# Kernel optimization log

Hardware: AMD Instinct MI355X
Metric: run time of the kernel (lower is better)

Reference implementation:

```python
import jax, jax.numpy as jnp
import numpy as np

# SCC (sliding/overlapping channel convolution) config, matching init_kwargs
C_IN = 64
C_OUT = 64
GRP_N = 8
OVERLAP = 4
G = C_IN // GRP_N          # input_grp_unit_dim = channels per sliding window = 8
STEP = G - OVERLAP         # channel stride between consecutive output channels = 4
B, H, W = 32, 128, 128


def setup_inputs() -> dict:
    key = jax.random.key(0)
    k1, k2 = jax.random.split(key)
    x = jax.random.normal(k1, (B, C_IN, H, W), dtype=jnp.float32)
    stdv = 1.0 / np.sqrt(G)  # reset_parameters: uniform(-stdv, stdv)
    weights = jax.random.uniform(k2, (C_OUT, G), dtype=jnp.float32,
                                 minval=-stdv, maxval=stdv)
    return {"x": x, "weights": weights}


def _expand_weights(weights):
    # Scatter the (C_OUT, G) sliding-window weights into a dense (C_OUT, C_IN)
    # channel-mixing matrix. Output channel o reads input channels
    # (o*STEP + j) % C_IN for j in [0, G). This keeps the irregular channel
    # access as a tiny scatter instead of materializing a (B,O,G,H,W) gather.
    o = jnp.arange(C_OUT)[:, None]            # (C_OUT, 1)
    j = jnp.arange(G)[None, :]                # (1, G)
    idx = (o * STEP + j) % C_IN               # (C_OUT, G) wrap-around window
    w_full = jnp.zeros((C_OUT, C_IN), dtype=weights.dtype)
    w_full = w_full.at[jnp.broadcast_to(o, idx.shape), idx].add(weights)
    return w_full


def reference(x, weights):
    w_full = _expand_weights(weights)                 # (C_OUT, C_IN)
    # 1x1 spatial conv == per-pixel channel contraction
    return jnp.einsum('oc,bchw->bohw', w_full, x)     # (B, C_OUT, H, W)
```

## Files before the change

kernel.cpp:

```cpp
#include <hip/hip_runtime.h>
#include <hip/hip_bf16.h>


#define CIN   64
#define COUT  64
#define GW    8
#define STEP  4
#define HW4   4096

__global__ __launch_bounds__(256) void scc_kernel(
    const float4* __restrict__ x,
    const float*  __restrict__ w,
    float4* __restrict__ out)
{
    __shared__ float4 wsv[COUT * 2];
    {
        float* ws = (float*)wsv;
        for (int i = threadIdx.x; i < COUT * GW; i += blockDim.x)
            ws[i] = w[i];
    }
    __syncthreads();

    int t   = blockIdx.x * blockDim.x + threadIdx.x;
    int b   = t >> 12;
    int hw4 = t & (HW4 - 1);

    const float4* xp = x   + ((long)b * CIN) * HW4 + hw4;
    float4*       op = out + ((long)b * COUT) * HW4 + hw4;

    float4 win[8];
#pragma unroll
    for (int k = 0; k < 8; ++k)
        win[k] = xp[(long)k * HW4];

#pragma unroll
    for (int wi = 0; wi < 16; ++wi) {
        float4 nxt[4];
        if (wi < 15) {
#pragma unroll
            for (int k = 0; k < 4; ++k) {
                int c = (4 * wi + 8 + k) & (CIN - 1);
                nxt[k] = xp[(long)c * HW4];
            }
        }

#pragma unroll
        for (int q = 0; q < 4; ++q) {
            int o = wi + 16 * q;
            float4 w0 = wsv[o * 2 + 0];
            float4 w1 = wsv[o * 2 + 1];
            float4 a;
            a.x = 0.f; a.y = 0.f; a.z = 0.f; a.w = 0.f;
#pragma unroll
            for (int j = 0; j < 8; ++j) {
                float wt = (j < 4) ? ((const float*)&w0)[j]
                                   : ((const float*)&w1)[j - 4];
                float4 xv = win[(4 * wi + j) & 7];
                a.x = fmaf(wt, xv.x, a.x);
                a.y = fmaf(wt, xv.y, a.y);
                a.z = fmaf(wt, xv.z, a.z);
                a.w = fmaf(wt, xv.w, a.w);
            }
            op[(long)o * HW4] = a;
        }

        if (wi < 15) {
#pragma unroll
            for (int k = 0; k < 4; ++k)
                win[(4 * wi + 8 + k) & 7] = nxt[k];
        }
    }
}

extern "C" void kernel_launch(void* const* d_in, const int* in_sizes, int n_in,
                              void* d_out, int out_size, void* d_ws, size_t ws_size,
                              hipStream_t stream) {
    const float4* x = (const float4*)d_in[0];
    const float*  w = (const float*)d_in[1];
    float4* out     = (float4*)d_out;

    const int total_vec = 32 * HW4;
    const int block = 256;
    const int grid  = total_vec / block;

    scc_kernel<<<grid, block, 0, stream>>>(x, w, out);
}
```

Before: 48.71 us.

## Split each pixel's output channels across four threads to raise parallelism

```diff
diff --git a/kernel.cpp b/kernel.cpp
--- a/kernel.cpp
+++ b/kernel.cpp
@@ -5,7 +5,6 @@
 #define CIN   64
 #define COUT  64
 #define GW    8
-#define STEP  4
 #define HW4   4096
 
 __global__ __launch_bounds__(256) void scc_kernel(
@@ -13,48 +12,44 @@
     const float*  __restrict__ w,
     float4* __restrict__ out)
 {
-    __shared__ float4 wsv[COUT * 2];
-    {
-        float* ws = (float*)wsv;
-        for (int i = threadIdx.x; i < COUT * GW; i += blockDim.x)
-            ws[i] = w[i];
-    }
+    __shared__ float ws[COUT * GW];
+    for (int i = threadIdx.x; i < COUT * GW; i += blockDim.x)
+        ws[i] = w[i];
     __syncthreads();
 
-    int t   = blockIdx.x * blockDim.x + threadIdx.x;
-    int b   = t >> 12;
-    int hw4 = t & (HW4 - 1);
+    const int tid = threadIdx.x;
+    const int q0  = tid >> 6;
+    const int pi  = blockIdx.x * 64 + (tid & 63);
+    const int b   = pi >> 12;
+    const int hw4 = pi & (HW4 - 1);
 
     const float4* xp = x   + ((long)b * CIN) * HW4 + hw4;
     float4*       op = out + ((long)b * COUT) * HW4 + hw4;
 
+    const int cbase = 16 * q0;
+
     float4 win[8];
 #pragma unroll
     for (int k = 0; k < 8; ++k)
-        win[k] = xp[(long)k * HW4];
+        win[k] = xp[(long)((cbase + k) & (CIN - 1)) * HW4];
 
 #pragma unroll
-    for (int wi = 0; wi < 16; ++wi) {
+    for (int wi = 0; wi < 4; ++wi) {
         float4 nxt[4];
-        if (wi < 15) {
+        if (wi < 3) {
 #pragma unroll
-            for (int k = 0; k < 4; ++k) {
-                int c = (4 * wi + 8 + k) & (CIN - 1);
-                nxt[k] = xp[(long)c * HW4];
-            }
+            for (int k = 0; k < 4; ++k)
+                nxt[k] = xp[(long)((cbase + 4 * wi + 8 + k) & (CIN - 1)) * HW4];
         }
 
 #pragma unroll
         for (int q = 0; q < 4; ++q) {
-            int o = wi + 16 * q;
-            float4 w0 = wsv[o * 2 + 0];
-            float4 w1 = wsv[o * 2 + 1];
+            int o = 4 * q0 + wi + 16 * q;
             float4 a;
             a.x = 0.f; a.y = 0.f; a.z = 0.f; a.w = 0.f;
 #pragma unroll
             for (int j = 0; j < 8; ++j) {
-                float wt = (j < 4) ? ((const float*)&w0)[j]
-                                   : ((const float*)&w1)[j - 4];
+                float wt  = ws[o * GW + j];
                 float4 xv = win[(4 * wi + j) & 7];
                 a.x = fmaf(wt, xv.x, a.x);
                 a.y = fmaf(wt, xv.y, a.y);
@@ -64,7 +59,7 @@
             op[(long)o * HW4] = a;
         }
 
-        if (wi < 15) {
+        if (wi < 3) {
 #pragma unroll
             for (int k = 0; k < 4; ++k)
                 win[(4 * wi + 8 + k) & 7] = nxt[k];
@@ -79,9 +74,8 @@
     const float*  w = (const float*)d_in[1];
     float4* out     = (float4*)d_out;
 
-    const int total_vec = 32 * HW4;
     const int block = 256;
-    const int grid  = total_vec / block;
+    const int grid  = 131072 / 64;
 
     scc_kernel<<<grid, block, 0, stream>>>(x, w, out);
 }
```

Result: slower. 51.82 us (+6.4%).
